# Kernel tuning notes

Hardware: AMD Instinct MI355X
Metric: run time of the kernel (lower is better)

The kernel has to match this reference:

```python
import jax, jax.numpy as jnp
import numpy as np

N_EMBD = 512
N_HEADS = 8
D_HEAD = N_EMBD // N_HEADS


def setup_inputs() -> dict:
    key = jax.random.key(0)
    k1, k2, k3, k4, k5 = jax.random.split(key, 5)
    B, T = 4, 2048
    scale = 1.0 / np.sqrt(N_EMBD)
    return {
        "x": jax.random.normal(k1, (B, T, N_EMBD), dtype=jnp.float32),
        # fused QKV projection: Linear(n_embd, 3*n_embd)
        "W_attn": jax.random.normal(k2, (N_EMBD, 3 * N_EMBD), dtype=jnp.float32) * scale,
        "b_attn": jax.random.normal(k3, (3 * N_EMBD,), dtype=jnp.float32) * 0.01,
        # output projection: Linear(n_embd, n_embd)
        "W_out": jax.random.normal(k4, (N_EMBD, N_EMBD), dtype=jnp.float32) * scale,
        "b_out": jax.random.normal(k5, (N_EMBD,), dtype=jnp.float32) * 0.01,
    }


def reference(x, W_attn, b_attn, W_out, b_out):
    B, T, C = x.shape
    # fused QKV projection then split
    qkv = x @ W_attn + b_attn  # [B, T, 3C]
    q, k, v = jnp.split(qkv, 3, axis=-1)
    # [B, T, C] -> [B, H, T, Dh]
    def heads(t):
        return t.reshape(B, T, N_HEADS, D_HEAD).transpose(0, 2, 1, 3)
    q, k, v = heads(q), heads(k), heads(v)
    # scaled dot-product attention (non-causal, no mask; dropout off in eval)
    scores = jnp.einsum("bhqd,bhkd->bhqk", q, k) / jnp.sqrt(jnp.float32(D_HEAD))
    attn = jax.nn.softmax(scores, axis=-1)
    y = jnp.einsum("bhqk,bhkd->bhqd", attn, v)  # [B, H, T, Dh]
    y = y.transpose(0, 2, 1, 3).reshape(B, T, C)
    # output projection (resid dropout off in eval)
    return y @ W_out + b_out
```

## Files before the change

kernel.cpp:

```cpp
#include <hip/hip_runtime.h>

typedef __attribute__((ext_vector_type(8))) short bf16x8;
typedef __attribute__((ext_vector_type(4))) float f32x4;
typedef unsigned short u16;
typedef unsigned int u32;

#define MFMA16(A, B, C) __builtin_amdgcn_mfma_f32_16x16x32_bf16((A), (B), (C), 0, 0, 0)

#if __has_builtin(__builtin_amdgcn_exp2f)
#define EXP2(x) __builtin_amdgcn_exp2f(x)
#else
#define EXP2(x) exp2f(x)
#endif

typedef __attribute__((address_space(3))) unsigned int lds_u32;
typedef const __attribute__((address_space(1))) unsigned int glb_u32;

__device__ __forceinline__ u16 f2bf(float f) {
  union { float f; unsigned u; } x; x.f = f;
  unsigned r = (x.u + 0x7fffu + ((x.u >> 16) & 1u)) >> 16;
  return (u16)r;
}
__device__ __forceinline__ float bf2f(u16 h) {
  union { float f; unsigned u; } x; x.u = ((unsigned)h) << 16;
  return x.f;
}

__device__ __forceinline__ void stage_sw64(const u16* src, u16* lds, int tid) {
#pragma unroll
  for (int i = 0; i < 2; i++) {
    int vv = tid + i * 256;
    int row = vv >> 3, c = vv & 7;
    const u16* gp = src + (size_t)row * 64 + (size_t)(c ^ (row & 7)) * 8;
    __builtin_amdgcn_global_load_lds((glb_u32*)gp,
        (lds_u32*)(lds + (size_t)(i * 256 + (tid & 192)) * 8), 16, 0, 0);
  }
}

template <int ROWS>
__device__ __forceinline__ void stage_ld512(const u16* src, u16* lds, int tid) {
#pragma unroll
  for (int i = 0; i < ROWS / 32; i++) {
    int vv = tid + i * 256;
    int row = vv >> 3, c = vv & 7;
    const u16* gp = src + (size_t)row * 512 + (size_t)(c ^ (row & 7)) * 8;
    __builtin_amdgcn_global_load_lds((glb_u32*)gp,
        (lds_u32*)(lds + (size_t)(i * 256 + (tid & 192)) * 8), 16, 0, 0);
  }
}

__global__ __launch_bounds__(256) void prep_kernel(const float* __restrict__ x,
                                                   u16* __restrict__ xb,
                                                   const float* __restrict__ Wa,
                                                   u16* __restrict__ wta,
                                                   const float* __restrict__ Wo,
                                                   u16* __restrict__ whi,
                                                   u16* __restrict__ wlo) {
  __shared__ u16 Th[64][72];
  __shared__ u16 Tl[64][72];
  const int bid = blockIdx.x;
  const int tid = threadIdx.x;

  if (bid < 4096) {
    int i = bid * 256 + tid;
    float4 v = ((const float4*)x)[i];
    ushort4 o;
    o.x = f2bf(v.x); o.y = f2bf(v.y); o.z = f2bf(v.z); o.w = f2bf(v.w);
    ((ushort4*)xb)[i] = o;
    return;
  }

  if (bid < 4288) {
    const int t = bid - 4096;
    const int n0 = (t % 24) * 64;
    const int k0 = (t / 24) * 64;
    const int r = tid >> 4, c4 = (tid & 15) * 4;
#pragma unroll
    for (int i = 0; i < 4; i++) {
      int row = r + i * 16;
      float4 v = *(const float4*)&Wa[(size_t)(k0 + row) * 1536 + n0 + c4];
      Th[c4 + 0][row] = f2bf(v.x);
      Th[c4 + 1][row] = f2bf(v.y);
      Th[c4 + 2][row] = f2bf(v.z);
      Th[c4 + 3][row] = f2bf(v.w);
    }
    __syncthreads();
    const int row = tid >> 2, c16 = (tid & 3) * 16;
    *(uint4*)&wta[(size_t)(n0 + row) * 512 + k0 + c16]     = *(uint4*)&Th[row][c16];
    *(uint4*)&wta[(size_t)(n0 + row) * 512 + k0 + c16 + 8] = *(uint4*)&Th[row][c16 + 8];
    return;
  }

  {
    const int t = bid - 4288;
    const int n0 = (t & 7) * 64;
    const int k0 = (t >> 3) * 64;
    const int r = tid >> 4, c4 = (tid & 15) * 4;
#pragma unroll
    for (int i = 0; i < 4; i++) {
      int row = r + i * 16;
      float4 v = *(const float4*)&Wo[(size_t)(k0 + row) * 512 + n0 + c4];
      float vv[4] = {v.x, v.y, v.z, v.w};
#pragma unroll
      for (int jj = 0; jj < 4; jj++) {
        u16 hi = f2bf(vv[jj]);
        Th[c4 + jj][row] = hi;
        Tl[c4 + jj][row] = f2bf(vv[jj] - bf2f(hi));
      }
    }
    __syncthreads();
    const int row = tid >> 2, c16 = (tid & 3) * 16;
    *(uint4*)&whi[(size_t)(n0 + row) * 512 + k0 + c16]     = *(uint4*)&Th[row][c16];
    *(uint4*)&whi[(size_t)(n0 + row) * 512 + k0 + c16 + 8] = *(uint4*)&Th[row][c16 + 8];
    *(uint4*)&wlo[(size_t)(n0 + row) * 512 + k0 + c16]     = *(uint4*)&Tl[row][c16];
    *(uint4*)&wlo[(size_t)(n0 + row) * 512 + k0 + c16 + 8] = *(uint4*)&Tl[row][c16 + 8];
  }
}

__global__ __launch_bounds__(256) void gemm_qkv(const u16* __restrict__ xb,
                                                const u16* __restrict__ wta,
                                                const float* __restrict__ b_attn,
                                                u16* __restrict__ q,
                                                u16* __restrict__ kk,
                                                u16* __restrict__ v) {
  __shared__ u16 Smem[18432];
  const int bid = blockIdx.x;
  const int xcd = bid & 7, rr = bid >> 3;
  const int m0 = (xcd * 8 + (rr & 7)) * 128;
  const int n0 = (rr >> 3) * 128;
  const int tid  = threadIdx.x;
  const int lane = tid & 63, w = tid >> 6;
  const int wm = w >> 1, wn = w & 1;
  const int quad = lane >> 4, l15 = lane & 15;
  const int sw0 = ((quad)     ^ (l15 & 7)) * 8;
  const int sw1 = ((quad + 4) ^ (l15 & 7)) * 8;

  f32x4 acc[4][4] = {};

  for (int kt = 0; kt < 8; kt++) {
    stage_ld512<128>(xb  + (size_t)m0 * 512 + kt * 64, Smem, tid);
    stage_ld512<128>(wta + (size_t)n0 * 512 + kt * 64, Smem + 8192, tid);
    __syncthreads();
#pragma unroll
    for (int ks = 0; ks < 2; ks++) {
      const int sw = ks ? sw1 : sw0;
      bf16x8 af[4], bf[4];
#pragma unroll
      for (int ri = 0; ri < 4; ri++)
        af[ri] = *(const bf16x8*)&Smem[(wm * 64 + ri * 16 + l15) * 64 + sw];
#pragma unroll
      for (int ci = 0; ci < 4; ci++)
        bf[ci] = *(const bf16x8*)&Smem[8192 + (wn * 64 + ci * 16 + l15) * 64 + sw];
#pragma unroll
      for (int ri = 0; ri < 4; ri++)
#pragma unroll
        for (int ci = 0; ci < 4; ci++)
          acc[ri][ci] = MFMA16(af[ri], bf[ci], acc[ri][ci]);
    }
    __syncthreads();
  }

  const float QS = 0.18033688011112043f;
  const int wave_n0 = n0 + wn * 64;
  const int chunk = wave_n0 >> 9;
  const int h = (wave_n0 & 511) >> 6;
  const int m_wave = m0 + wm * 64;
  const int b = m_wave >> 11, t0 = m_wave & 2047;
  const int bh = b * 8 + h;

  if (chunk < 2) {
    u16* T = Smem + w * 4608;
    u16* dst = (chunk == 0) ? q : kk;
    const float scale = (chunk == 0) ? QS : 1.0f;
#pragma unroll
    for (int ri = 0; ri < 4; ri++)
#pragma unroll
      for (int ci = 0; ci < 4; ci++) {
        float bias = b_attn[wave_n0 + ci * 16 + l15];
#pragma unroll
        for (int r = 0; r < 4; r++) {
          int tl = ri * 16 + quad * 4 + r;
          T[tl * 72 + ci * 16 + l15] = f2bf((acc[ri][ci][r] + bias) * scale);
        }
      }
    u16* gdst = dst + (size_t)(bh * 2048 + t0 + lane) * 64;
#pragma unroll
    for (int j = 0; j < 8; j++)
      *(uint4*)&gdst[j * 8] = *(const uint4*)&T[lane * 72 + j * 8];
  } else {
#pragma unroll
    for (int ri = 0; ri < 4; ri++)
#pragma unroll
      for (int ci = 0; ci < 4; ci++) {
        int n = wave_n0 + ci * 16 + l15;
        float bias = b_attn[n];
        int d = n & 63;
        int tv = t0 + ri * 16 + quad * 4;
        int it = tv >> 7, ks2 = (tv >> 5) & 3, qd = (tv >> 3) & 3, jj = tv & 7;
        ushort4 pk;
        pk.x = f2bf(acc[ri][ci][0] + bias);
        pk.y = f2bf(acc[ri][ci][1] + bias);
        pk.z = f2bf(acc[ri][ci][2] + bias);
        pk.w = f2bf(acc[ri][ci][3] + bias);
        size_t idx = ((((size_t)bh * 16 + it) * 4 + ks2) * 64 + d) * 32 + qd * 8 + jj;
        *(ushort4*)&v[idx] = pk;
      }
  }
}

__global__ __launch_bounds__(256, 4) void flash_attn(const u16* __restrict__ q,
                                                     const u16* __restrict__ k,
                                                     const u16* __restrict__ vt,
                                                     u16* __restrict__ yb) {
  __shared__ u16 K_lds[2][64 * 64];
  __shared__ u16 P_lds[4 * 2 * 16 * 72];

  const int flat = blockIdx.y * 16 + blockIdx.x;
  const int bh = (flat & 7) * 4 + ((flat >> 3) & 3);
  const int qt = flat >> 5;

  const int tid  = threadIdx.x;
  const int lane = tid & 63, w = tid >> 6;
  const int quad = lane >> 4, l15 = lane & 15;
  const int sw0 = ((quad)     ^ (l15 & 7)) * 8;
  const int sw1 = ((quad + 4) ^ (l15 & 7)) * 8;

  const u16* qp = q  + (size_t)bh * 131072;
  const u16* kp = k  + (size_t)bh * 131072;
  const u16* vp = vt + (size_t)bh * 131072;

  bf16x8 qf[2];
#pragma unroll
  for (int ks = 0; ks < 2; ks++)
    qf[ks] = *(const bf16x8*)(qp + (size_t)(qt * 64 + w * 16 + l15) * 64 + ks * 32 + quad * 8);

  f32x4 l_acc = {};
  f32x4 o[4] = {};

  bf16x8 ones;
  {
    short one = (short)0x3F80;
    ones = (bf16x8){one, one, one, one, one, one, one, one};
  }

  u16* Pw = &P_lds[w * 2 * 16 * 72];

#define S_PHASE(KB, PB)                                                        \
  do {                                                                         \
    _Pragma("unroll")                                                          \
    for (int jt = 0; jt < 4; jt++) {                                           \
      bf16x8 kf0 = *(const bf16x8*)&(KB)[(jt * 16 + l15) * 64 + sw0];          \
      bf16x8 kf1 = *(const bf16x8*)&(KB)[(jt * 16 + l15) * 64 + sw1];          \
      f32x4 s = {0.f, 0.f, 0.f, 0.f};                                          \
      s = MFMA16(kf0, qf[0], s);                                               \
      s = MFMA16(kf1, qf[1], s);                                               \
      u32 pb[4];                                                               \
      _Pragma("unroll")                                                        \
      for (int r = 0; r < 4; r++) pb[r] = __float_as_uint(EXP2(s[r]));         \
      uint2 pk;                                                                \
      pk.x = __builtin_amdgcn_perm(pb[1], pb[0], 0x07060302u);                 \
      pk.y = __builtin_amdgcn_perm(pb[3], pb[2], 0x07060302u);                 \
      *(uint2*)&(PB)[l15 * 72 + jt * 16 + quad * 4] = pk;                      \
    }                                                                          \
  } while (0)

#define PV_PHASE(VIT, PB)                                                      \
  do {                                                                         \
    bf16x8 vf[2][4];                                                           \
    _Pragma("unroll")                                                          \
    for (int dt = 0; dt < 4; dt++)                                             \
      vf[0][dt] = *(const bf16x8*)((VIT) + (dt * 16 + l15) * 32 + quad * 8);   \
    _Pragma("unroll")                                                          \
    for (int dt = 0; dt < 4; dt++)                                             \
      vf[1][dt] = *(const bf16x8*)((VIT) + 2048 + (dt * 16 + l15) * 32 + quad * 8); \
    __builtin_amdgcn_s_setprio(1);                                             \
    _Pragma("unroll")                                                          \
    for (int ks = 0; ks < 2; ks++) {                                           \
      bf16x8 pf = *(const bf16x8*)&(PB)[l15 * 72 + ks * 32 + quad * 8];        \
      l_acc = MFMA16(pf, ones, l_acc);                                         \
      _Pragma("unroll")                                                        \
      for (int dt = 0; dt < 4; dt++)                                           \
        o[dt] = MFMA16(pf, vf[ks][dt], o[dt]);                                 \
    }                                                                          \
    __builtin_amdgcn_s_setprio(0);                                             \
  } while (0)

  stage_sw64(kp, K_lds[0], tid);
  stage_sw64(kp + 4096, K_lds[1], tid);
  __syncthreads();
  S_PHASE(K_lds[0], Pw);

  for (int it = 0; it < 31; it++) {
    __syncthreads();
    if (it < 30) stage_sw64(kp + (size_t)(it + 2) * 4096, K_lds[it & 1], tid);
    u16* Pc = Pw + (it & 1) * 16 * 72;
    u16* Pn = Pw + ((it + 1) & 1) * 16 * 72;
    S_PHASE(K_lds[(it + 1) & 1], Pn);
    PV_PHASE(vp + (it) * 4096, Pc);
  }
  PV_PHASE(vp + 31 * 4096, Pw + (31 & 1) * 16 * 72);

#undef S_PHASE
#undef PV_PHASE

  const int b = bh >> 3, h = bh & 7;
  u32* Tw = (u32*)Pw;
#pragma unroll
  for (int r = 0; r < 4; r++) {
    float inv = 1.f / l_acc[r];
#pragma unroll
    for (int dt = 0; dt < 4; dt++) {
      float val = o[dt][r] * inv;
      u16 hi = f2bf(val);
      u16 lo = f2bf(val - bf2f(hi));
      Tw[(quad * 4 + r) * 68 + dt * 16 + l15] = (u32)hi | ((u32)lo << 16);
    }
  }
  {
    int t = qt * 64 + w * 16 + l15;
    size_t rowb = (size_t)(b * 2048 + t) * 512 + h * 64 + quad * 16;
    uint4 g0 = *(uint4*)&Tw[l15 * 68 + quad * 16 + 0];
    uint4 g1 = *(uint4*)&Tw[l15 * 68 + quad * 16 + 4];
    uint4 g2 = *(uint4*)&Tw[l15 * 68 + quad * 16 + 8];
    uint4 g3 = *(uint4*)&Tw[l15 * 68 + quad * 16 + 12];
    uint4 hi4, lo4;
    hi4.x = __builtin_amdgcn_perm(g0.y, g0.x, 0x05040100u);
    hi4.y = __builtin_amdgcn_perm(g0.w, g0.z, 0x05040100u);
    hi4.z = __builtin_amdgcn_perm(g1.y, g1.x, 0x05040100u);
    hi4.w = __builtin_amdgcn_perm(g1.w, g1.z, 0x05040100u);
    lo4.x = __builtin_amdgcn_perm(g0.y, g0.x, 0x07060302u);
    lo4.y = __builtin_amdgcn_perm(g0.w, g0.z, 0x07060302u);
    lo4.z = __builtin_amdgcn_perm(g1.y, g1.x, 0x07060302u);
    lo4.w = __builtin_amdgcn_perm(g1.w, g1.z, 0x07060302u);
    *(uint4*)&yb[rowb] = hi4;
    *(uint4*)&yb[(size_t)4 * 2048 * 512 + rowb] = lo4;
    hi4.x = __builtin_amdgcn_perm(g2.y, g2.x, 0x05040100u);
    hi4.y = __builtin_amdgcn_perm(g2.w, g2.z, 0x05040100u);
    hi4.z = __builtin_amdgcn_perm(g3.y, g3.x, 0x05040100u);
    hi4.w = __builtin_amdgcn_perm(g3.w, g3.z, 0x05040100u);
    lo4.x = __builtin_amdgcn_perm(g2.y, g2.x, 0x07060302u);
    lo4.y = __builtin_amdgcn_perm(g2.w, g2.z, 0x07060302u);
    lo4.z = __builtin_amdgcn_perm(g3.y, g3.x, 0x07060302u);
    lo4.w = __builtin_amdgcn_perm(g3.w, g3.z, 0x07060302u);
    *(uint4*)&yb[rowb + 8] = hi4;
    *(uint4*)&yb[(size_t)4 * 2048 * 512 + rowb + 8] = lo4;
  }
}

__global__ __launch_bounds__(256) void gemm_out(const u16* __restrict__ yhi,
                                                const u16* __restrict__ ylo,
                                                const u16* __restrict__ whi,
                                                const u16* __restrict__ wlo,
                                                const float* __restrict__ b_out,
                                                float* __restrict__ out) {
  __shared__ u16 Ah[128 * 64];
  __shared__ u16 Al[128 * 64];
  __shared__ u16 Bh[64 * 64];
  __shared__ u16 Bl[64 * 64];
  const int bid = blockIdx.x;
  const int xcd = bid & 7, rr = bid >> 3;
  const int m0 = (xcd * 8 + (rr & 7)) * 128;
  const int n0 = (rr >> 3) * 64;
  const int tid  = threadIdx.x;
  const int lane = tid & 63, w = tid >> 6;
  const int wm = w >> 1, wn = w & 1;
  const int quad = lane >> 4, l15 = lane & 15;
  const int sw0 = ((quad)     ^ (l15 & 7)) * 8;
  const int sw1 = ((quad + 4) ^ (l15 & 7)) * 8;

  f32x4 acc[4][2] = {};

  for (int kt = 0; kt < 8; kt++) {
    const int k0 = kt * 64;
    stage_ld512<128>(yhi + (size_t)m0 * 512 + k0, Ah, tid);
    stage_ld512<128>(ylo + (size_t)m0 * 512 + k0, Al, tid);
    stage_ld512<64>(whi + (size_t)n0 * 512 + k0, Bh, tid);
    stage_ld512<64>(wlo + (size_t)n0 * 512 + k0, Bl, tid);
    __syncthreads();
#pragma unroll
    for (int ks = 0; ks < 2; ks++) {
      const int sw = ks ? sw1 : sw0;
      bf16x8 afh[4], afl[4], bfh[2], bfl[2];
#pragma unroll
      for (int ri = 0; ri < 4; ri++) {
        afh[ri] = *(const bf16x8*)&Ah[(wm * 64 + ri * 16 + l15) * 64 + sw];
        afl[ri] = *(const bf16x8*)&Al[(wm * 64 + ri * 16 + l15) * 64 + sw];
      }
#pragma unroll
      for (int ci = 0; ci < 2; ci++) {
        bfh[ci] = *(const bf16x8*)&Bh[(wn * 32 + ci * 16 + l15) * 64 + sw];
        bfl[ci] = *(const bf16x8*)&Bl[(wn * 32 + ci * 16 + l15) * 64 + sw];
      }
#pragma unroll
      for (int ri = 0; ri < 4; ri++)
#pragma unroll
        for (int ci = 0; ci < 2; ci++) {
          acc[ri][ci] = MFMA16(afh[ri], bfh[ci], acc[ri][ci]);
          acc[ri][ci] = MFMA16(afh[ri], bfl[ci], acc[ri][ci]);
          acc[ri][ci] = MFMA16(afl[ri], bfh[ci], acc[ri][ci]);
        }
    }
    __syncthreads();
  }

#pragma unroll
  for (int ri = 0; ri < 4; ri++) {
#pragma unroll
    for (int ci = 0; ci < 2; ci++) {
      int n = n0 + wn * 32 + ci * 16 + l15;
      float bias = b_out[n];
#pragma unroll
      for (int r = 0; r < 4; r++) {
        int m = m0 + wm * 64 + ri * 16 + quad * 4 + r;
        out[(size_t)m * 512 + n] = acc[ri][ci][r] + bias;
      }
    }
  }
}

extern "C" void kernel_launch(void* const* d_in, const int* in_sizes, int n_in,
                              void* d_out, int out_size, void* d_ws, size_t ws_size,
                              hipStream_t stream) {
  const float* x      = (const float*)d_in[0];
  const float* W_attn = (const float*)d_in[1];
  const float* b_attn = (const float*)d_in[2];
  const float* W_out  = (const float*)d_in[3];
  const float* b_out  = (const float*)d_in[4];
  float* out = (float*)d_out;

  char* ws = (char*)d_ws;
  u16* xb   = (u16*)(ws + 0);
  u16* wta  = (u16*)(ws + 8388608);
  u16* wtoh = (u16*)(ws + 9961472);
  u16* wtol = (u16*)(ws + 10485760);
  u16* qb   = (u16*)(ws + 11010048);
  u16* kb   = (u16*)(ws + 19398656);
  u16* vtb  = (u16*)(ws + 27787264);
  u16* yhi  = (u16*)(ws + 36175872);

  prep_kernel<<<4352, 256, 0, stream>>>(x, xb, W_attn, wta, W_out, wtoh, wtol);
  gemm_qkv<<<768, 256, 0, stream>>>(xb, wta, b_attn, qb, kb, vtb);
  flash_attn<<<dim3(16, 64), 256, 0, stream>>>(qb, kb, vtb, yhi);
  gemm_out<<<512, 256, 0, stream>>>(yhi, yhi + (size_t)4 * 2048 * 512, wtoh, wtol, b_out, out);
}
```

Measured before the change: 193.3 us.

## Stage V tiles in LDS and simplify flash loop to a single-stage schedule

```diff
diff --git a/kernel.cpp b/kernel.cpp
--- a/kernel.cpp
+++ b/kernel.cpp
@@ -32,6 +32,15 @@
     int vv = tid + i * 256;
     int row = vv >> 3, c = vv & 7;
     const u16* gp = src + (size_t)row * 64 + (size_t)(c ^ (row & 7)) * 8;
+    __builtin_amdgcn_global_load_lds((glb_u32*)gp,
+        (lds_u32*)(lds + (size_t)(i * 256 + (tid & 192)) * 8), 16, 0, 0);
+  }
+}
+
+__device__ __forceinline__ void stage_lin64(const u16* src, u16* lds, int tid) {
+#pragma unroll
+  for (int i = 0; i < 2; i++) {
+    const u16* gp = src + (size_t)(i * 256 + tid) * 8;
     __builtin_amdgcn_global_load_lds((glb_u32*)gp,
         (lds_u32*)(lds + (size_t)(i * 256 + (tid & 192)) * 8), 16, 0, 0);
   }
@@ -212,8 +221,9 @@
                                                      const u16* __restrict__ k,
                                                      const u16* __restrict__ vt,
                                                      u16* __restrict__ yb) {
-  __shared__ u16 K_lds[2][64 * 64];
-  __shared__ u16 P_lds[4 * 2 * 16 * 72];
+  __shared__ u16 Kb[2][64 * 64];
+  __shared__ u16 Vb[2][64 * 64];
+  __shared__ u16 P_lds[4 * 16 * 64];
 
   const int flat = blockIdx.y * 16 + blockIdx.x;
   const int bh = (flat & 7) * 4 + ((flat >> 3) & 3);
@@ -243,68 +253,56 @@
     ones = (bf16x8){one, one, one, one, one, one, one, one};
   }
 
-  u16* Pw = &P_lds[w * 2 * 16 * 72];
-
-#define S_PHASE(KB, PB)                                                        \
-  do {                                                                         \
-    _Pragma("unroll")                                                          \
-    for (int jt = 0; jt < 4; jt++) {                                           \
-      bf16x8 kf0 = *(const bf16x8*)&(KB)[(jt * 16 + l15) * 64 + sw0];          \
-      bf16x8 kf1 = *(const bf16x8*)&(KB)[(jt * 16 + l15) * 64 + sw1];          \
-      f32x4 s = {0.f, 0.f, 0.f, 0.f};                                          \
-      s = MFMA16(kf0, qf[0], s);                                               \
-      s = MFMA16(kf1, qf[1], s);                                               \
-      u32 pb[4];                                                               \
-      _Pragma("unroll")                                                        \
-      for (int r = 0; r < 4; r++) pb[r] = __float_as_uint(EXP2(s[r]));         \
-      uint2 pk;                                                                \
-      pk.x = __builtin_amdgcn_perm(pb[1], pb[0], 0x07060302u);                 \
-      pk.y = __builtin_amdgcn_perm(pb[3], pb[2], 0x07060302u);                 \
-      *(uint2*)&(PB)[l15 * 72 + jt * 16 + quad * 4] = pk;                      \
-    }                                                                          \
-  } while (0)
-
-#define PV_PHASE(VIT, PB)                                                      \
-  do {                                                                         \
-    bf16x8 vf[2][4];                                                           \
-    _Pragma("unroll")                                                          \
-    for (int dt = 0; dt < 4; dt++)                                             \
-      vf[0][dt] = *(const bf16x8*)((VIT) + (dt * 16 + l15) * 32 + quad * 8);   \
-    _Pragma("unroll")                                                          \
-    for (int dt = 0; dt < 4; dt++)                                             \
-      vf[1][dt] = *(const bf16x8*)((VIT) + 2048 + (dt * 16 + l15) * 32 + quad * 8); \
-    __builtin_amdgcn_s_setprio(1);                                             \
-    _Pragma("unroll")                                                          \
-    for (int ks = 0; ks < 2; ks++) {                                           \
-      bf16x8 pf = *(const bf16x8*)&(PB)[l15 * 72 + ks * 32 + quad * 8];        \
-      l_acc = MFMA16(pf, ones, l_acc);                                         \
-      _Pragma("unroll")                                                        \
-      for (int dt = 0; dt < 4; dt++)                                           \
-        o[dt] = MFMA16(pf, vf[ks][dt], o[dt]);                                 \
-    }                                                                          \
-    __builtin_amdgcn_s_setprio(0);                                             \
-  } while (0)
-
-  stage_sw64(kp, K_lds[0], tid);
-  stage_sw64(kp + 4096, K_lds[1], tid);
+  u16* Pw = &P_lds[w * 1024];
+  const int psw = l15 & 7;
+
+  stage_sw64(kp, Kb[0], tid);
+  stage_lin64(vp, Vb[0], tid);
+
+  for (int it = 0; it < 32; it++) {
+    __syncthreads();
+    if (it < 31) {
+      stage_sw64(kp + (size_t)(it + 1) * 4096, Kb[(it + 1) & 1], tid);
+      stage_lin64(vp + (size_t)(it + 1) * 4096, Vb[(it + 1) & 1], tid);
+    }
+    const u16* Kc = Kb[it & 1];
+    const u16* Vc = Vb[it & 1];
+
+#pragma unroll
+    for (int jt = 0; jt < 4; jt++) {
+      bf16x8 kf0 = *(const bf16x8*)&Kc[(jt * 16 + l15) * 64 + sw0];
+      bf16x8 kf1 = *(const bf16x8*)&Kc[(jt * 16 + l15) * 64 + sw1];
+      f32x4 s = {0.f, 0.f, 0.f, 0.f};
+      s = MFMA16(kf0, qf[0], s);
+      s = MFMA16(kf1, qf[1], s);
+      u32 pb[4];
+#pragma unroll
+      for (int r = 0; r < 4; r++) pb[r] = __float_as_uint(EXP2(s[r]));
+      uint2 pk;
+      pk.x = __builtin_amdgcn_perm(pb[1], pb[0], 0x07060302u);
+      pk.y = __builtin_amdgcn_perm(pb[3], pb[2], 0x07060302u);
+      int c = jt * 2 + (quad >> 1);
+      *(uint2*)&Pw[l15 * 64 + ((c ^ psw) << 3) + (quad & 1) * 4] = pk;
+    }
+
+    __builtin_amdgcn_s_setprio(1);
+#pragma unroll
+    for (int ks = 0; ks < 2; ks++) {
+      bf16x8 pf = *(const bf16x8*)&Pw[l15 * 64 + (((ks * 4 + quad) ^ psw) << 3)];
+      l_acc = MFMA16(pf, ones, l_acc);
+#pragma unroll
+      for (int dt = 0; dt < 4; dt++) {
+        bf16x8 vf = *(const bf16x8*)&Vc[ks * 2048 + (dt * 16 + l15) * 32 + quad * 8];
+        o[dt] = MFMA16(pf, vf, o[dt]);
+      }
+    }
+    __builtin_amdgcn_s_setprio(0);
+  }
+
   __syncthreads();
-  S_PHASE(K_lds[0], Pw);
-
-  for (int it = 0; it < 31; it++) {
-    __syncthreads();
-    if (it < 30) stage_sw64(kp + (size_t)(it + 2) * 4096, K_lds[it & 1], tid);
-    u16* Pc = Pw + (it & 1) * 16 * 72;
-    u16* Pn = Pw + ((it + 1) & 1) * 16 * 72;
-    S_PHASE(K_lds[(it + 1) & 1], Pn);
-    PV_PHASE(vp + (it) * 4096, Pc);
-  }
-  PV_PHASE(vp + 31 * 4096, Pw + (31 & 1) * 16 * 72);
-
-#undef S_PHASE
-#undef PV_PHASE
 
   const int b = bh >> 3, h = bh & 7;
-  u32* Tw = (u32*)Pw;
+  u32* Tw = (u32*)(&Kb[0][0]) + (size_t)w * 1088;
 #pragma unroll
   for (int r = 0; r < 4; r++) {
     float inv = 1.f / l_acc[r];
```

New measurement: 175.5 us. 1.1x faster.
